# Performance work log

Measured on AMD Instinct MI355X. Metric: run time of the kernel, lower is better.

Reference implementation:

```python
import jax, jax.numpy as jnp
import numpy as np

ATOM_DIM, HID, N_LAYERS, N_HEADS, PF_DIM = 34, 256, 2, 8, 1024
B, NA, NP = 32, 512, 1024


def setup_inputs() -> dict:
    key = jax.random.key(0)
    ks = iter(jax.random.split(key, 32))
    def rn(shape, s=0.02):
        return jax.random.normal(next(ks), shape, dtype=jnp.float32) * s
    L = N_LAYERS
    z = lambda *s: jnp.zeros(s, jnp.float32)
    return {
        "trg": jax.random.normal(next(ks), (B, NA, ATOM_DIM), dtype=jnp.float32),
        "src": jax.random.normal(next(ks), (B, NP, HID), dtype=jnp.float32),
        "ft_w": rn((HID, ATOM_DIM)), "ft_b": z(HID),
        "ln_g": jnp.ones((L, HID), jnp.float32), "ln_b": z(L, HID),
        "sa_wq": rn((L, HID, HID)), "sa_bq": z(L, HID),
        "sa_wk": rn((L, HID, HID)), "sa_bk": z(L, HID),
        "sa_wv": rn((L, HID, HID)), "sa_bv": z(L, HID),
        "sa_wf": rn((L, HID, HID)), "sa_bf": z(L, HID),
        "ea_wq": rn((L, HID, HID)), "ea_bq": z(L, HID),
        "ea_wk": rn((L, HID, HID)), "ea_bk": z(L, HID),
        "ea_wv": rn((L, HID, HID)), "ea_bv": z(L, HID),
        "ea_wf": rn((L, HID, HID)), "ea_bf": z(L, HID),
        "pf_w1": rn((L, PF_DIM, HID)), "pf_b1": z(L, PF_DIM),
        "pf_w2": rn((L, HID, PF_DIM)), "pf_b2": z(L, HID),
        "fc1_w": rn((256, HID)), "fc1_b": z(256),
        "fc2_w": rn((2, 256)), "fc2_b": z(2),
    }


def _ln(x, g, b, eps=1e-5):
    m = jnp.mean(x, axis=-1, keepdims=True)
    v = jnp.mean(jnp.square(x - m), axis=-1, keepdims=True)
    return (x - m) * jax.lax.rsqrt(v + eps) * g + b


def _attn(xq, xkv, wq, bq, wk, bk, wv, bv, wf, bf):
    b_, lq, h = xq.shape
    d = h // N_HEADS
    q = (xq @ wq.T + bq).reshape(b_, lq, N_HEADS, d).transpose(0, 2, 1, 3)
    k = (xkv @ wk.T + bk).reshape(b_, -1, N_HEADS, d).transpose(0, 2, 1, 3)
    v = (xkv @ wv.T + bv).reshape(b_, -1, N_HEADS, d).transpose(0, 2, 1, 3)
    scale = jnp.sqrt(jnp.float32(d))  # TransformerCPI: sqrt(hid_dim // n_heads)
    a = jax.nn.softmax(jnp.einsum('bhqd,bhkd->bhqk', q, k) / scale, axis=-1)
    o = jnp.einsum('bhqk,bhkd->bhqd', a, v).transpose(0, 2, 1, 3).reshape(b_, lq, h)
    return o @ wf.T + bf


def reference(trg, src, ft_w, ft_b, ln_g, ln_b,
              sa_wq, sa_bq, sa_wk, sa_bk, sa_wv, sa_bv, sa_wf, sa_bf,
              ea_wq, ea_bq, ea_wk, ea_bk, ea_wv, ea_bv, ea_wf, ea_bf,
              pf_w1, pf_b1, pf_w2, pf_b2, fc1_w, fc1_b, fc2_w, fc2_b):
    x = trg @ ft_w.T + ft_b  # [B, NA, HID]
    for l in range(N_LAYERS):
        x = _ln(x + _attn(x, x, sa_wq[l], sa_bq[l], sa_wk[l], sa_bk[l],
                          sa_wv[l], sa_bv[l], sa_wf[l], sa_bf[l]), ln_g[l], ln_b[l])
        x = _ln(x + _attn(x, src, ea_wq[l], ea_bq[l], ea_wk[l], ea_bk[l],
                          ea_wv[l], ea_bv[l], ea_wf[l], ea_bf[l]), ln_g[l], ln_b[l])
        h = jax.nn.relu(x @ pf_w1[l].T + pf_b1[l]) @ pf_w2[l].T + pf_b2[l]
        x = _ln(x + h, ln_g[l], ln_b[l])
    # norm-weighted attention pooling (replaces the nested Python loops)
    w = jax.nn.softmax(jnp.linalg.norm(x, axis=2), axis=1)  # [B, NA]
    pooled = jnp.einsum('bn,bnh->bh', w, x)  # [B, HID]
    return jax.nn.relu(pooled @ fc1_w.T + fc1_b) @ fc2_w.T + fc2_b
```

## Files before the change

### kernel.cpp

```cpp
#include <hip/hip_runtime.h>
#include <hip/hip_bf16.h>
#include <math.h>

#define B_   32
#define NA   512
#define NP   1024
#define HID  256
#define NH   8
#define DH   32
#define PF   1024

typedef short bf16x8 __attribute__((ext_vector_type(8)));
typedef float f32x4  __attribute__((ext_vector_type(4)));
typedef float f32x16 __attribute__((ext_vector_type(16)));
typedef unsigned u32x4 __attribute__((ext_vector_type(4)));

#define ZERO16 {0.f,0.f,0.f,0.f,0.f,0.f,0.f,0.f,0.f,0.f,0.f,0.f,0.f,0.f,0.f,0.f}

static __device__ inline unsigned short f2bf(float f) {
    __hip_bfloat16 h = __float2bfloat16(f);
    unsigned short u;
    __builtin_memcpy(&u, &h, 2);
    return u;
}
static __device__ inline unsigned cvtpk(float lo, float hi) {
    return (unsigned)f2bf(lo) | ((unsigned)f2bf(hi) << 16);
}
static __device__ inline bf16x8 pack8(float4 a, float4 b) {
    bf16x8 r;
    r[0] = (short)f2bf(a.x); r[1] = (short)f2bf(a.y);
    r[2] = (short)f2bf(a.z); r[3] = (short)f2bf(a.w);
    r[4] = (short)f2bf(b.x); r[5] = (short)f2bf(b.y);
    r[6] = (short)f2bf(b.z); r[7] = (short)f2bf(b.w);
    return r;
}

__global__ __launch_bounds__(256) void ft_kernel(const float* __restrict__ trg,
    const float* __restrict__ w, const float* __restrict__ b,
    float* __restrict__ out, unsigned short* __restrict__ outb)
{
    __shared__ float Ws[256][35];
    int tid = threadIdx.x;
    for (int k = 0; k < 34; ++k) Ws[tid][k] = w[tid*34 + k];
    float bias = b[tid];
    __syncthreads();
    int m0 = blockIdx.x * 32;
    for (int r = 0; r < 32; ++r) {
        int m = m0 + r;
        const float* tr = trg + (size_t)m*34;
        float acc = bias;
        #pragma unroll
        for (int k = 0; k < 34; ++k) acc += tr[k] * Ws[tid][k];
        out [(size_t)m*HID + tid] = acc;
        outb[(size_t)m*HID + tid] = f2bf(acc);
    }
}

__global__ __launch_bounds__(256) void cvt_bf16(const float* __restrict__ in,
    unsigned short* __restrict__ outb, int n8)
{
    int i = blockIdx.x*256 + threadIdx.x;
    int stride = gridDim.x*256;
    for (; i < n8; i += stride) {
        float4 a = *(const float4*)(in + (size_t)i*8);
        float4 b = *(const float4*)(in + (size_t)i*8 + 4);
        *(bf16x8*)(outb + (size_t)i*8) = pack8(a, b);
    }
}

__global__ __launch_bounds__(256) void cvt_w(
    const float* __restrict__ s0, const float* __restrict__ s1,
    const float* __restrict__ s2, const float* __restrict__ s3,
    const float* __restrict__ s4, const float* __restrict__ s5,
    const float* __restrict__ s6, const float* __restrict__ s7,
    const float* __restrict__ s8, const float* __restrict__ s9,
    unsigned short* __restrict__ dst)
{
    const int z = blockIdx.z;
    const float* src;
    switch (z) {
        case 0: src = s0; break; case 1: src = s1; break;
        case 2: src = s2; break; case 3: src = s3; break;
        case 4: src = s4; break; case 5: src = s5; break;
        case 6: src = s6; break; case 7: src = s7; break;
        case 8: src = s8; break; default: src = s9; break;
    }
    const int n8 = (z < 8) ? 16384 : 65536;
    const size_t off = (z < 8) ? (size_t)z*131072 : (1048576u + (size_t)(z-8)*524288);
    unsigned short* o = dst + off;
    int i = blockIdx.x*256 + threadIdx.x;
    const int stride = gridDim.x*256;
    for (; i < n8; i += stride) {
        float4 a = *(const float4*)(src + (size_t)i*8);
        float4 b = *(const float4*)(src + (size_t)i*8 + 4);
        *(bf16x8*)(o + (size_t)i*8) = pack8(a, b);
    }
}

static __device__ inline void gemm_core(const unsigned short* __restrict__ Ab,
    const unsigned short* __restrict__ Wb, const float* __restrict__ bias,
    void* __restrict__ Cv, int M, int N, int K, int mode, int L, float oscale,
    int bx, int by)
{
    __shared__ __attribute__((aligned(16))) unsigned short As[128][72];
    __shared__ __attribute__((aligned(16))) unsigned short Bs[64][72];
    const int tid = threadIdx.x;
    const int wave = tid >> 6, lane = tid & 63, lq = lane & 15, g = lane >> 4;
    const int wr = wave >> 1, wc = wave & 1;
    const int m0 = by * 128, n0 = bx * 64;

    const int ar = tid >> 1, ac = (tid & 1) * 32;
    const int br = tid >> 2, bc = (tid & 3) * 16;

    f32x4 acc[4][2] = {};
    bf16x8 sa[4], sw[2];

    auto LOAD = [&](int kt) {
        const int k0 = kt * 64;
        const unsigned short* Ap = Ab + (size_t)(m0 + ar)*K + k0 + ac;
        #pragma unroll
        for (int i = 0; i < 4; ++i)
            sa[i] = *(const bf16x8*)(Ap + i*8);
        const unsigned short* Wp = Wb + (size_t)(n0 + br)*K + k0 + bc;
        #pragma unroll
        for (int i = 0; i < 2; ++i)
            sw[i] = *(const bf16x8*)(Wp + i*8);
    };
    auto STORE = [&]() {
        #pragma unroll
        for (int i = 0; i < 4; ++i) *(bf16x8*)&As[ar][ac + i*8] = sa[i];
        #pragma unroll
        for (int i = 0; i < 2; ++i) *(bf16x8*)&Bs[br][bc + i*8] = sw[i];
    };

    const int nk = K / 64;
    LOAD(0);
    for (int kt = 0; kt < nk; ++kt) {
        __syncthreads();
        STORE();
        __syncthreads();
        if (kt + 1 < nk) LOAD(kt + 1);
        #pragma unroll
        for (int ks = 0; ks < 2; ++ks) {
            bf16x8 bf0 = *(const bf16x8*)&Bs[wc*32 +  0 + lq][ks*32 + g*8];
            bf16x8 bf1 = *(const bf16x8*)&Bs[wc*32 + 16 + lq][ks*32 + g*8];
            #pragma unroll
            for (int i = 0; i < 4; ++i) {
                bf16x8 af = *(const bf16x8*)&As[wr*64 + i*16 + lq][ks*32 + g*8];
                acc[i][0] = __builtin_amdgcn_mfma_f32_16x16x32_bf16(af, bf0, acc[i][0], 0, 0, 0);
                acc[i][1] = __builtin_amdgcn_mfma_f32_16x16x32_bf16(af, bf1, acc[i][1], 0, 0, 0);
            }
        }
    }

    float bb[2];
    #pragma unroll
    for (int j = 0; j < 2; ++j) bb[j] = bias[n0 + wc*32 + j*16 + lq];

    #pragma unroll
    for (int i = 0; i < 4; ++i) {
        const int mb = m0 + wr*64 + i*16 + 4*g;
        #pragma unroll
        for (int j = 0; j < 2; ++j) {
            const int n = n0 + wc*32 + j*16 + lq;
            f32x4 v = acc[i][j];
            #pragma unroll
            for (int r = 0; r < 4; ++r) v[r] = (v[r] + bb[j]) * oscale;
            if (mode == 0) {
                float* Cf = (float*)Cv;
                #pragma unroll
                for (int r = 0; r < 4; ++r) Cf[(size_t)(mb + r)*N + n] = v[r];
            } else if (mode == 1) {
                unsigned short* Cb = (unsigned short*)Cv;
                #pragma unroll
                for (int r = 0; r < 4; ++r) Cb[(size_t)(mb + r)*N + n] = f2bf(v[r]);
            } else if (mode == 3) {
                unsigned short* Cb = (unsigned short*)Cv;
                #pragma unroll
                for (int r = 0; r < 4; ++r) Cb[(size_t)(mb + r)*N + n] = f2bf(fmaxf(v[r], 0.f));
            } else if (mode == 4) {
                unsigned short* Cb = (unsigned short*)Cv;
                const int bI = mb / L, kk = mb % L;
                const int hh = n >> 5, d = n & 31;
                const int t2 = kk >> 5, dc = d >> 4, hi2 = (d >> 3) & 1;
                unsigned short* base = Cb
                    + ((size_t)(((bI*NH + hh)*(L >> 5) + t2)*2 + dc))*512
                    + ((kk & 31) + 32*hi2)*8 + (d & 7);
                base[0]  = f2bf(v[0]); base[8]  = f2bf(v[1]);
                base[16] = f2bf(v[2]); base[24] = f2bf(v[3]);
            } else {
                unsigned short* Cb = (unsigned short*)Cv;
                const int bI = mb / L, kk = mb % L;
                const int hh = n >> 5, d = n & 31;
                const int t = kk >> 6, oct = (kk >> 3) & 7;
                const int c = oct >> 1, hiV = oct & 1;
                ushort4 pk;
                pk.x = f2bf(v[0]); pk.y = f2bf(v[1]); pk.z = f2bf(v[2]); pk.w = f2bf(v[3]);
                *(ushort4*)(Cb
                    + ((size_t)(((bI*NH + hh)*(L >> 6) + t)*4 + c))*512
                    + (d + 32*hiV)*8 + (kk & 7)) = pk;
            }
        }
    }
}

__global__ __launch_bounds__(256) void gemm_mfma(const unsigned short* __restrict__ A,
    const unsigned short* __restrict__ W, const float* __restrict__ bias,
    void* __restrict__ C, int M, int N, int K, int mode, int L)
{
    gemm_core(A, W, bias, C, M, N, K, mode, L, 1.f, blockIdx.x, blockIdx.y);
}

__global__ __launch_bounds__(256) void qkv_mfma(const unsigned short* __restrict__ Aq,
    const unsigned short* __restrict__ Akv,
    const unsigned short* __restrict__ Wq, const float* __restrict__ bq,
    const unsigned short* __restrict__ Wk, const float* __restrict__ bk,
    const unsigned short* __restrict__ Wv, const float* __restrict__ bv,
    void* __restrict__ qo, void* __restrict__ ko, void* __restrict__ vo,
    int Mq, int Mkv, int L)
{
    const int z = blockIdx.z;
    const unsigned short* A = (z == 0) ? Aq : Akv;
    const unsigned short* W = (z == 0) ? Wq : ((z == 1) ? Wk : Wv);
    const float* bb = (z == 0) ? bq : ((z == 1) ? bk : bv);
    void* C = (z == 0) ? qo : ((z == 1) ? ko : vo);
    const int M = (z == 0) ? Mq : Mkv;
    const int mode = (z == 0) ? 1 : ((z == 1) ? 4 : 5);
    const float sc = (z == 0) ? 0.25504082364238727f : 1.f;
    if ((int)blockIdx.y * 128 >= M) return;
    gemm_core(A, W, bb, C, M, HID, HID, mode, L, sc, blockIdx.x, blockIdx.y);
}

__global__ __launch_bounds__(256) void attn_mfma(const unsigned short* __restrict__ Qb,
    const unsigned short* __restrict__ KF, const unsigned short* __restrict__ VF,
    unsigned short* __restrict__ O, int Lk)
{
    __shared__ float Ll[4][32];
    const int orig = blockIdx.x;
    const int sw = (orig & 7) * 128 + (orig >> 3);
    const int qt = sw & 3;
    const int h  = (sw >> 2) & 7;
    const int b  = sw >> 5;
    const int tid = threadIdx.x, w = tid >> 6, lane = tid & 63;
    const int q32 = lane & 31, hi = lane >> 5;

    const unsigned short* qp = Qb + ((size_t)(b*NA + qt*128 + w*32 + q32))*HID + h*DH + hi*8;
    bf16x8 qf0 = *(const bf16x8*)qp;
    bf16x8 qf1 = *(const bf16x8*)(qp + 16);

    const unsigned short* Kf = KF + (size_t)((b*NH + h)*(Lk >> 5)*2)*512 + lane*8;
    const unsigned short* Vf = VF + (size_t)((b*NH + h)*(Lk >> 6)*4)*512 + lane*8;

    f32x16 o_acc = ZERO16;
    float lacc = 0.f;

    bf16x8 kfA[4], kfB[4], vfT[4];
    auto LOADK = [&](int t, bf16x8* kd) {
        #pragma unroll
        for (int f = 0; f < 4; ++f)
            kd[f] = *(const bf16x8*)(Kf + (size_t)(t*4 + f)*512);
    };
    auto STEP = [&](const bf16x8* kf, int t) {
        #pragma unroll
        for (int c = 0; c < 4; ++c)
            vfT[c] = *(const bf16x8*)(Vf + (size_t)(t*4 + c)*512);
        f32x16 st0 = ZERO16, st1 = ZERO16;
        st0 = __builtin_amdgcn_mfma_f32_32x32x16_bf16(kf[0], qf0, st0, 0, 0, 0);
        st0 = __builtin_amdgcn_mfma_f32_32x32x16_bf16(kf[1], qf1, st0, 0, 0, 0);
        st1 = __builtin_amdgcn_mfma_f32_32x32x16_bf16(kf[2], qf0, st1, 0, 0, 0);
        st1 = __builtin_amdgcn_mfma_f32_32x32x16_bf16(kf[3], qf1, st1, 0, 0, 0);
        bf16x8 pa[4];
        float lp = 0.f;
        #pragma unroll
        for (int c = 0; c < 4; ++c) {
            const f32x16& s = (c < 2) ? st0 : st1;
            const int rb = (c & 1) * 8;
            float p0 = __builtin_amdgcn_exp2f(s[rb+0]);
            float p1 = __builtin_amdgcn_exp2f(s[rb+1]);
            float p2 = __builtin_amdgcn_exp2f(s[rb+2]);
            float p3 = __builtin_amdgcn_exp2f(s[rb+3]);
            float p4 = __builtin_amdgcn_exp2f(s[rb+4]);
            float p5 = __builtin_amdgcn_exp2f(s[rb+5]);
            float p6 = __builtin_amdgcn_exp2f(s[rb+6]);
            float p7 = __builtin_amdgcn_exp2f(s[rb+7]);
            lp += (p0+p1) + (p2+p3) + (p4+p5) + (p6+p7);
            unsigned A1 = cvtpk(p0, p1), A2 = cvtpk(p2, p3);
            unsigned B1 = cvtpk(p4, p5), B2 = cvtpk(p6, p7);
            auto r1 = __builtin_amdgcn_permlane32_swap(A1, B1, false, false);
            auto r2 = __builtin_amdgcn_permlane32_swap(A2, B2, false, false);
            u32x4 pw; pw[0] = r1[0]; pw[1] = r2[0]; pw[2] = r1[1]; pw[3] = r2[1];
            __builtin_memcpy(&pa[c], &pw, 16);
        }
        lacc += lp;
        #pragma unroll
        for (int c = 0; c < 4; ++c)
            o_acc = __builtin_amdgcn_mfma_f32_32x32x16_bf16(pa[c], vfT[c], o_acc, 0, 0, 0);
    };

    const int nt = Lk >> 6;
    LOADK(0, kfA);
    for (int t = 0; t < nt; t += 2) {
        LOADK(t + 1, kfB);
        STEP(kfA, t);
        if (t + 2 < nt) LOADK(t + 2, kfA);
        STEP(kfB, t + 1);
    }

    float lt = lacc + __shfl_xor(lacc, 32);
    float linv = 1.f / lt;
    if (hi == 0) Ll[w][q32] = linv;
    f32x4 li[4];
    #pragma unroll
    for (int jg = 0; jg < 4; ++jg) li[jg] = *(const f32x4*)&Ll[w][jg*8 + hi*4];

    unsigned short* Op = O + ((size_t)(b*NA + qt*128 + w*32))*HID + h*DH + q32;
    #pragma unroll
    for (int jg = 0; jg < 4; ++jg) {
        #pragma unroll
        for (int r2 = 0; r2 < 4; ++r2) {
            const int q = jg*8 + hi*4 + r2;
            Op[(size_t)q*HID] = f2bf(o_acc[jg*4 + r2] * li[jg][r2]);
        }
    }
}

__global__ __launch_bounds__(256) void add_ln(float* __restrict__ x,
    const float* __restrict__ t, const float* __restrict__ g,
    const float* __restrict__ bt, unsigned short* __restrict__ xb)
{
    const int row = blockIdx.x*4 + (threadIdx.x >> 6);
    const int lane = threadIdx.x & 63;
    const size_t base = (size_t)row*HID + lane*4;
    float4 v = *(const float4*)(x + base);
    float4 tv = *(const float4*)(t + base);
    v.x += tv.x; v.y += tv.y; v.z += tv.z; v.w += tv.w;
    float s = v.x + v.y + v.z + v.w;
    #pragma unroll
    for (int o = 32; o > 0; o >>= 1) s += __shfl_xor(s, o);
    float mean = s * (1.f/256.f);
    float4 d = {v.x - mean, v.y - mean, v.z - mean, v.w - mean};
    float q2 = d.x*d.x + d.y*d.y + d.z*d.z + d.w*d.w;
    #pragma unroll
    for (int o = 32; o > 0; o >>= 1) q2 += __shfl_xor(q2, o);
    float rs = rsqrtf(q2*(1.f/256.f) + 1e-5f);
    float4 gv = *(const float4*)(g + lane*4);
    float4 bv = *(const float4*)(bt + lane*4);
    float4 ov;
    ov.x = d.x*rs*gv.x + bv.x; ov.y = d.y*rs*gv.y + bv.y;
    ov.z = d.z*rs*gv.z + bv.z; ov.w = d.w*rs*gv.w + bv.w;
    *(float4*)(x + base) = ov;
    ushort4 pk;
    pk.x = f2bf(ov.x); pk.y = f2bf(ov.y); pk.z = f2bf(ov.z); pk.w = f2bf(ov.w);
    *(ushort4*)(xb + base) = pk;
}

__global__ __launch_bounds__(256) void norms_k(const float* __restrict__ x,
    float* __restrict__ nw)
{
    const int row = blockIdx.x*4 + (threadIdx.x >> 6);
    const int lane = threadIdx.x & 63;
    float4 v = *(const float4*)(x + (size_t)row*HID + lane*4);
    float s = v.x*v.x + v.y*v.y + v.z*v.z + v.w*v.w;
    #pragma unroll
    for (int o = 32; o > 0; o >>= 1) s += __shfl_xor(s, o);
    if (lane == 0) nw[row] = sqrtf(s);
}

__global__ __launch_bounds__(256) void pooled_k(const float* __restrict__ x,
    const float* __restrict__ nw, float* __restrict__ pooled)
{
    __shared__ float sw[NA];
    __shared__ float red[256];
    __shared__ float part[8][33];
    const int b = blockIdx.x, hc = blockIdx.y;
    const int tid = threadIdx.x;
    const float* nb = nw + (size_t)b*NA;
    float v0 = nb[tid], v1 = nb[tid + 256];
    red[tid] = fmaxf(v0, v1); __syncthreads();
    for (int s = 128; s > 0; s >>= 1) { if (tid < s) red[tid] = fmaxf(red[tid], red[tid+s]); __syncthreads(); }
    float mx = red[0]; __syncthreads();
    float e0 = __expf(v0 - mx), e1 = __expf(v1 - mx);
    sw[tid] = e0; sw[tid + 256] = e1;
    red[tid] = e0 + e1; __syncthreads();
    for (int s = 128; s > 0; s >>= 1) { if (tid < s) red[tid] += red[tid+s]; __syncthreads(); }
    float inv = 1.f / red[0];
    __syncthreads();
    const int ng = tid >> 5, col = tid & 31;
    const float* xp = x + (size_t)b*NA*HID + hc*32 + col;
    float acc = 0.f;
    for (int n = ng; n < NA; n += 8)
        acc += sw[n] * xp[(size_t)n*HID];
    part[ng][col] = acc;
    __syncthreads();
    if (tid < 32) {
        float s = 0.f;
        #pragma unroll
        for (int i = 0; i < 8; ++i) s += part[i][tid];
        pooled[(size_t)b*HID + hc*32 + tid] = s * inv;
    }
}

__global__ __launch_bounds__(256) void head_k(const float* __restrict__ pooled,
    const float* __restrict__ fc1w, const float* __restrict__ fc1b,
    const float* __restrict__ fc2w, const float* __restrict__ fc2b,
    float* __restrict__ out)
{
    __shared__ float p[HID];
    __shared__ float a1[HID];
    const int b = blockIdx.x, tid = threadIdx.x;
    p[tid] = pooled[(size_t)b*HID + tid];
    __syncthreads();
    float s1 = fc1b[tid];
    const float* w1 = fc1w + (size_t)tid*HID;
    for (int k2 = 0; k2 < HID; k2 += 4) {
        float4 w = *(const float4*)(w1 + k2);
        s1 += p[k2]*w.x + p[k2+1]*w.y + p[k2+2]*w.z + p[k2+3]*w.w;
    }
    a1[tid] = fmaxf(s1, 0.f);
    __syncthreads();
    if (tid < 2) {
        float s2 = fc2b[tid];
        const float* w2 = fc2w + (size_t)tid*HID;
        for (int k2 = 0; k2 < HID; ++k2) s2 += a1[k2] * w2[k2];
        out[b*2 + tid] = s2;
    }
}

extern "C" void kernel_launch(void* const* d_in, const int* in_sizes, int n_in,
                              void* d_out, int out_size, void* d_ws, size_t ws_size,
                              hipStream_t stream)
{
    const float* trg  = (const float*)d_in[0];
    const float* src  = (const float*)d_in[1];
    const float* ft_w = (const float*)d_in[2];
    const float* ft_b = (const float*)d_in[3];
    const float* ln_g = (const float*)d_in[4];
    const float* ln_b = (const float*)d_in[5];
    const float* sa_wq = (const float*)d_in[6];  const float* sa_bq = (const float*)d_in[7];
    const float* sa_wk = (const float*)d_in[8];  const float* sa_bk = (const float*)d_in[9];
    const float* sa_wv = (const float*)d_in[10]; const float* sa_bv = (const float*)d_in[11];
    const float* sa_wf = (const float*)d_in[12]; const float* sa_bf = (const float*)d_in[13];
    const float* ea_wq = (const float*)d_in[14]; const float* ea_bq = (const float*)d_in[15];
    const float* ea_wk = (const float*)d_in[16]; const float* ea_bk = (const float*)d_in[17];
    const float* ea_wv = (const float*)d_in[18]; const float* ea_bv = (const float*)d_in[19];
    const float* ea_wf = (const float*)d_in[20]; const float* ea_bf = (const float*)d_in[21];
    const float* pf_w1 = (const float*)d_in[22]; const float* pf_b1 = (const float*)d_in[23];
    const float* pf_w2 = (const float*)d_in[24]; const float* pf_b2 = (const float*)d_in[25];
    const float* fc1w  = (const float*)d_in[26]; const float* fc1b  = (const float*)d_in[27];
    const float* fc2w  = (const float*)d_in[28]; const float* fc2b  = (const float*)d_in[29];
    float* out = (float*)d_out;

    const size_t NTOK = (size_t)B_*NA;
    const size_t NSRC = (size_t)B_*NP;
    float* ws = (float*)d_ws;
    float* x  = ws;
    float* u  = x + NTOK*HID;
    float* nw = u + NTOK*HID;
    float* pooled = nw + NTOK;
    unsigned short* xb   = (unsigned short*)(pooled + B_*HID);
    unsigned short* tb   = xb + NTOK*HID;
    unsigned short* srcb = tb + NTOK*HID;
    unsigned short* qb   = srcb + NSRC*HID;
    unsigned short* kb   = qb + NTOK*HID;
    unsigned short* vTb  = kb + NSRC*HID;
    unsigned short* wb   = vTb + NSRC*HID;
    unsigned short* hb   = qb;

    unsigned short* saq_b = wb;
    unsigned short* sak_b = wb +  131072;
    unsigned short* sav_b = wb +  262144;
    unsigned short* saf_b = wb +  393216;
    unsigned short* eaq_b = wb +  524288;
    unsigned short* eak_b = wb +  655360;
    unsigned short* eav_b = wb +  786432;
    unsigned short* eaf_b = wb +  917504;
    unsigned short* pw1_b = wb + 1048576;
    unsigned short* pw2_b = wb + 1572864;

    const int M = (int)NTOK;
    dim3 blk(256);

    cvt_w<<<dim3(64, 1, 10), blk, 0, stream>>>(sa_wq, sa_wk, sa_wv, sa_wf,
        ea_wq, ea_wk, ea_wv, ea_wf, pf_w1, pf_w2, wb);
    ft_kernel<<<M/32, blk, 0, stream>>>(trg, ft_w, ft_b, x, xb);
    cvt_bf16<<<1024, blk, 0, stream>>>(src, srcb, (int)(NSRC*HID/8));

    for (int l = 0; l < 2; ++l) {
        const size_t wo = (size_t)l*HID*HID, bo = (size_t)l*HID;
        qkv_mfma<<<dim3(HID/64, M/128, 3), blk, 0, stream>>>(xb, xb,
            saq_b+wo, sa_bq+bo, sak_b+wo, sa_bk+bo, sav_b+wo, sa_bv+bo,
            qb, kb, vTb, M, M, NA);
        attn_mfma<<<dim3(1024), blk, 0, stream>>>(qb, kb, vTb, tb, NA);
        gemm_mfma<<<dim3(HID/64, M/128), blk, 0, stream>>>(tb, saf_b+wo, sa_bf+bo, u, M, HID, HID, 0, 0);
        add_ln<<<M/4, blk, 0, stream>>>(x, u, ln_g+bo, ln_b+bo, xb);
        qkv_mfma<<<dim3(HID/64, (int)NSRC/128, 3), blk, 0, stream>>>(xb, srcb,
            eaq_b+wo, ea_bq+bo, eak_b+wo, ea_bk+bo, eav_b+wo, ea_bv+bo,
            qb, kb, vTb, M, (int)NSRC, NP);
        attn_mfma<<<dim3(1024), blk, 0, stream>>>(qb, kb, vTb, tb, NP);
        gemm_mfma<<<dim3(HID/64, M/128), blk, 0, stream>>>(tb, eaf_b+wo, ea_bf+bo, u, M, HID, HID, 0, 0);
        add_ln<<<M/4, blk, 0, stream>>>(x, u, ln_g+bo, ln_b+bo, xb);
        gemm_mfma<<<dim3(PF/64, M/128), blk, 0, stream>>>(xb, pw1_b+(size_t)l*PF*HID, pf_b1+(size_t)l*PF, hb, M, PF, HID, 3, 0);
        gemm_mfma<<<dim3(HID/64, M/128), blk, 0, stream>>>(hb, pw2_b+(size_t)l*HID*PF, pf_b2+bo, u, M, HID, PF, 0, 0);
        add_ln<<<M/4, blk, 0, stream>>>(x, u, ln_g+bo, ln_b+bo, xb);
    }

    norms_k<<<M/4, blk, 0, stream>>>(x, nw);
    pooled_k<<<dim3(B_, 8), blk, 0, stream>>>(x, nw, pooled);
    head_k<<<B_, blk, 0, stream>>>(pooled, fc1w, fc1b, fc2w, fc2b, out);
}
```

Measured before the change: 489.9 us.

## Widen GEMM tiles to 128x128 with fragment-ordered LDS and XCD block swizzle

The GEMM core now computes 128x128 output tiles instead of 128x64, so each wave issues 16 MFMAs per k-step instead of 8 and reuses each loaded A fragment across four B fragments. Shared memory is stored pre-arranged in MFMA fragment order, so each lane reads one contiguous 16-byte chunk without padding. Block indices are remapped so neighbouring tiles land on the same XCD for better L2 reuse. The trade-off is half as many blocks (fewer waves in flight on a 256-CU part) and higher accumulator register pressure.

```diff
diff --git a/kernel.cpp b/kernel.cpp
--- a/kernel.cpp
+++ b/kernel.cpp
@@ -102,35 +102,36 @@
     void* __restrict__ Cv, int M, int N, int K, int mode, int L, float oscale,
     int bx, int by)
 {
-    __shared__ __attribute__((aligned(16))) unsigned short As[128][72];
-    __shared__ __attribute__((aligned(16))) unsigned short Bs[64][72];
+    __shared__ __attribute__((aligned(16))) unsigned short Af[16*64*8];
+    __shared__ __attribute__((aligned(16))) unsigned short Wf[16*64*8];
     const int tid = threadIdx.x;
     const int wave = tid >> 6, lane = tid & 63, lq = lane & 15, g = lane >> 4;
     const int wr = wave >> 1, wc = wave & 1;
-    const int m0 = by * 128, n0 = bx * 64;
+    const int m0 = by * 128, n0 = bx * 128;
 
     const int ar = tid >> 1, ac = (tid & 1) * 32;
-    const int br = tid >> 2, bc = (tid & 3) * 16;
-
-    f32x4 acc[4][2] = {};
-    bf16x8 sa[4], sw[2];
+    const int fbase = (ar >> 4)*2 + (tid & 1);
+    const int lslot = ar & 15;
+
+    f32x4 acc[4][4] = {};
+    bf16x8 sa[4], sw[4];
 
     auto LOAD = [&](int kt) {
         const int k0 = kt * 64;
         const unsigned short* Ap = Ab + (size_t)(m0 + ar)*K + k0 + ac;
         #pragma unroll
-        for (int i = 0; i < 4; ++i)
-            sa[i] = *(const bf16x8*)(Ap + i*8);
-        const unsigned short* Wp = Wb + (size_t)(n0 + br)*K + k0 + bc;
-        #pragma unroll
-        for (int i = 0; i < 2; ++i)
-            sw[i] = *(const bf16x8*)(Wp + i*8);
+        for (int i = 0; i < 4; ++i) sa[i] = *(const bf16x8*)(Ap + i*8);
+        const unsigned short* Wp = Wb + (size_t)(n0 + ar)*K + k0 + ac;
+        #pragma unroll
+        for (int i = 0; i < 4; ++i) sw[i] = *(const bf16x8*)(Wp + i*8);
     };
     auto STORE = [&]() {
         #pragma unroll
-        for (int i = 0; i < 4; ++i) *(bf16x8*)&As[ar][ac + i*8] = sa[i];
-        #pragma unroll
-        for (int i = 0; i < 2; ++i) *(bf16x8*)&Bs[br][bc + i*8] = sw[i];
+        for (int i = 0; i < 4; ++i)
+            *(bf16x8*)&Af[((size_t)fbase*64 + lslot + 16*i)*8] = sa[i];
+        #pragma unroll
+        for (int i = 0; i < 4; ++i)
+            *(bf16x8*)&Wf[((size_t)fbase*64 + lslot + 16*i)*8] = sw[i];
     };
 
     const int nk = K / 64;
@@ -142,27 +143,30 @@
         if (kt + 1 < nk) LOAD(kt + 1);
         #pragma unroll
         for (int ks = 0; ks < 2; ++ks) {
-            bf16x8 bf0 = *(const bf16x8*)&Bs[wc*32 +  0 + lq][ks*32 + g*8];
-            bf16x8 bf1 = *(const bf16x8*)&Bs[wc*32 + 16 + lq][ks*32 + g*8];
+            bf16x8 bfr[4];
+            #pragma unroll
+            for (int j = 0; j < 4; ++j)
+                bfr[j] = *(const bf16x8*)&Wf[((size_t)(((wc*4+j)*2+ks)*64) + lane)*8];
             #pragma unroll
             for (int i = 0; i < 4; ++i) {
-                bf16x8 af = *(const bf16x8*)&As[wr*64 + i*16 + lq][ks*32 + g*8];
-                acc[i][0] = __builtin_amdgcn_mfma_f32_16x16x32_bf16(af, bf0, acc[i][0], 0, 0, 0);
-                acc[i][1] = __builtin_amdgcn_mfma_f32_16x16x32_bf16(af, bf1, acc[i][1], 0, 0, 0);
+                bf16x8 af = *(const bf16x8*)&Af[((size_t)(((wr*4+i)*2+ks)*64) + lane)*8];
+                #pragma unroll
+                for (int j = 0; j < 4; ++j)
+                    acc[i][j] = __builtin_amdgcn_mfma_f32_16x16x32_bf16(af, bfr[j], acc[i][j], 0, 0, 0);
             }
         }
     }
 
-    float bb[2];
-    #pragma unroll
-    for (int j = 0; j < 2; ++j) bb[j] = bias[n0 + wc*32 + j*16 + lq];
+    float bb[4];
+    #pragma unroll
+    for (int j = 0; j < 4; ++j) bb[j] = bias[n0 + wc*64 + j*16 + lq];
 
     #pragma unroll
     for (int i = 0; i < 4; ++i) {
         const int mb = m0 + wr*64 + i*16 + 4*g;
         #pragma unroll
-        for (int j = 0; j < 2; ++j) {
-            const int n = n0 + wc*32 + j*16 + lq;
+        for (int j = 0; j < 4; ++j) {
+            const int n = n0 + wc*64 + j*16 + lq;
             f32x4 v = acc[i][j];
             #pragma unroll
             for (int r = 0; r < 4; ++r) v[r] = (v[r] + bb[j]) * oscale;
@@ -204,11 +208,19 @@
     }
 }
 
+static __device__ inline void xcd_swz(int d, int nx, int nxy, int& bx, int& by)
+{
+    const int w = (d & 7) * (nxy >> 3) + (d >> 3);
+    bx = w % nx; by = w / nx;
+}
+
 __global__ __launch_bounds__(256) void gemm_mfma(const unsigned short* __restrict__ A,
     const unsigned short* __restrict__ W, const float* __restrict__ bias,
     void* __restrict__ C, int M, int N, int K, int mode, int L)
 {
-    gemm_core(A, W, bias, C, M, N, K, mode, L, 1.f, blockIdx.x, blockIdx.y);
+    int bx, by;
+    xcd_swz(blockIdx.y*gridDim.x + blockIdx.x, gridDim.x, gridDim.x*gridDim.y, bx, by);
+    gemm_core(A, W, bias, C, M, N, K, mode, L, 1.f, bx, by);
 }
 
 __global__ __launch_bounds__(256) void qkv_mfma(const unsigned short* __restrict__ Aq,
@@ -227,8 +239,10 @@
     const int M = (z == 0) ? Mq : Mkv;
     const int mode = (z == 0) ? 1 : ((z == 1) ? 4 : 5);
     const float sc = (z == 0) ? 0.25504082364238727f : 1.f;
-    if ((int)blockIdx.y * 128 >= M) return;
-    gemm_core(A, W, bb, C, M, HID, HID, mode, L, sc, blockIdx.x, blockIdx.y);
+    int bx, by;
+    xcd_swz(blockIdx.y*gridDim.x + blockIdx.x, gridDim.x, gridDim.x*gridDim.y, bx, by);
+    if (by * 128 >= M) return;
+    gemm_core(A, W, bb, C, M, HID, HID, mode, L, sc, bx, by);
 }
 
 __global__ __launch_bounds__(256) void attn_mfma(const unsigned short* __restrict__ Qb,
@@ -487,20 +501,20 @@
 
     for (int l = 0; l < 2; ++l) {
         const size_t wo = (size_t)l*HID*HID, bo = (size_t)l*HID;
-        qkv_mfma<<<dim3(HID/64, M/128, 3), blk, 0, stream>>>(xb, xb,
+        qkv_mfma<<<dim3(HID/128, M/128, 3), blk, 0, stream>>>(xb, xb,
             saq_b+wo, sa_bq+bo, sak_b+wo, sa_bk+bo, sav_b+wo, sa_bv+bo,
             qb, kb, vTb, M, M, NA);
         attn_mfma<<<dim3(1024), blk, 0, stream>>>(qb, kb, vTb, tb, NA);
-        gemm_mfma<<<dim3(HID/64, M/128), blk, 0, stream>>>(tb, saf_b+wo, sa_bf+bo, u, M, HID, HID, 0, 0);
+        gemm_mfma<<<dim3(HID/128, M/128), blk, 0, stream>>>(tb, saf_b+wo, sa_bf+bo, u, M, HID, HID, 0, 0);
         add_ln<<<M/4, blk, 0, stream>>>(x, u, ln_g+bo, ln_b+bo, xb);
-        qkv_mfma<<<dim3(HID/64, (int)NSRC/128, 3), blk, 0, stream>>>(xb, srcb,
+        qkv_mfma<<<dim3(HID/128, (int)NSRC/128, 3), blk, 0, stream>>>(xb, srcb,
             eaq_b+wo, ea_bq+bo, eak_b+wo, ea_bk+bo, eav_b+wo, ea_bv+bo,
             qb, kb, vTb, M, (int)NSRC, NP);
         attn_mfma<<<dim3(1024), blk, 0, stream>>>(qb, kb, vTb, tb, NP);
-        gemm_mfma<<<dim3(HID/64, M/128), blk, 0, stream>>>(tb, eaf_b+wo, ea_bf+bo, u, M, HID, HID, 0, 0);
+        gemm_mfma<<<dim3(HID/128, M/128), blk, 0, stream>>>(tb, eaf_b+wo, ea_bf+bo, u, M, HID, HID, 0, 0);
         add_ln<<<M/4, blk, 0, stream>>>(x, u, ln_g+bo, ln_b+bo, xb);
-        gemm_mfma<<<dim3(PF/64, M/128), blk, 0, stream>>>(xb, pw1_b+(size_t)l*PF*HID, pf_b1+(size_t)l*PF, hb, M, PF, HID, 3, 0);
-        gemm_mfma<<<dim3(HID/64, M/128), blk, 0, stream>>>(hb, pw2_b+(size_t)l*HID*PF, pf_b2+bo, u, M, HID, PF, 0, 0);
+        gemm_mfma<<<dim3(PF/128, M/128), blk, 0, stream>>>(xb, pw1_b+(size_t)l*PF*HID, pf_b1+(size_t)l*PF, hb, M, PF, HID, 3, 0);
+        gemm_mfma<<<dim3(HID/128, M/128), blk, 0, stream>>>(hb, pw2_b+(size_t)l*HID*PF, pf_b2+bo, u, M, HID, PF, 0, 0);
         add_ln<<<M/4, blk, 0, stream>>>(x, u, ln_g+bo, ln_b+bo, xb);
     }
 
```

After: 565.9 us. 1.16x slower.
